# Optimization experiments

Hardware: AMD Instinct MI355X
Metric: run time of the kernel (lower is better)

The kernel has to match this reference:

```python
import jax, jax.numpy as jnp
import numpy as np
from math import factorial

MAXL = 5
TAUS = [8, 8, 8, 8, 8, 8]
OUT_TAUS = [8, 8, 8, 8, 8, 8]
BM_EPS = 1e-5
BATCH = 1024


def _cg_coeff(l1, l2, l, m1, m2, m):
    # Standard Clebsch-Gordan coefficient <l1 m1 l2 m2 | l m> (Racah formula).
    if m1 + m2 != m:
        return 0.0
    f = factorial
    pre = ((2 * l + 1) * f(l + l1 - l2) * f(l - l1 + l2) * f(l1 + l2 - l) / f(l1 + l2 + l + 1)) ** 0.5
    pre *= (f(l + m) * f(l - m) * f(l1 - m1) * f(l1 + m1) * f(l2 - m2) * f(l2 + m2)) ** 0.5
    s = 0.0
    for k in range(0, l1 + l2 - l + 1):
        ds = [k, l1 + l2 - l - k, l1 - m1 - k, l2 + m2 - k, l - l2 + m1 + k, l - l1 - m2 + k]
        if min(ds) < 0:
            continue
        d = 1.0
        for v in ds:
            d *= f(v)
        s += (-1.0) ** k / d
    return pre * s


def _cg_block(l1, l2, l):
    C = np.zeros((2 * l + 1, 2 * l1 + 1, 2 * l2 + 1), dtype=np.float32)
    for m in range(-l, l + 1):
        for m1 in range(-l1, l1 + 1):
            m2 = m - m1
            if -l2 <= m2 <= l2:
                C[m + l, m1 + l1, m2 + l2] = _cg_coeff(l1, l2, l, m1, m2, m)
    return C


# Triple enumeration order matches cal_middle_taus (l1 outer, l2, then l).
TRIPLES = []
for _l1 in range(MAXL + 1):
    for _l2 in range(_l1 + 1):
        for _l in range(_l1 - _l2, min(_l1 + _l2, MAXL) + 1):
            TRIPLES.append((_l1, _l2, _l))
CG_BLOCKS = [jnp.asarray(_cg_block(*t)) for t in TRIPLES]

MIDDLE_TAUS = np.zeros(MAXL + 1, dtype=np.int64)
for (_l1, _l2, _l) in TRIPLES:
    MIDDLE_TAUS[_l] += TAUS[_l1] * TAUS[_l2]
IN_LEN = int(sum(TAUS[l] * (2 * l + 1) for l in range(MAXL + 1)))    # 288
OUT_LEN = int(sum(OUT_TAUS[l] * (2 * l + 1) for l in range(MAXL + 1)))  # 288
WLEN = int(sum(OUT_TAUS[l] * int(MIDDLE_TAUS[l]) for l in range(MAXL + 1)))  # 35328
STD_LEN = int(MIDDLE_TAUS.sum())  # 4416


def _forward(activations, weights, moving_std):
    B = activations.shape[0]
    act = activations[..., 0] + 1j * activations[..., 1]  # [B, IN_LEN] complex64
    # split into per-degree blocks F[l]: [B, tau_l, 2l+1]
    F = []
    st = 0
    for l in range(MAXL + 1):
        n = TAUS[l] * (2 * l + 1)
        F.append(act[:, st:st + n].reshape(B, TAUS[l], 2 * l + 1))
        st += n
    # CG tensor product: one fragment per (l1,l2,l) triple, grouped by output degree l
    mids = [[] for _ in range(MAXL + 1)]
    for (l1, l2, l), C in zip(TRIPLES, CG_BLOCKS):
        frag = jnp.einsum('mac,bta,bsc->btsm', C.astype(act.dtype), F[l1], F[l2])
        mids[l].append(frag.reshape(B, TAUS[l1] * TAUS[l2], 2 * l + 1))
    # per-fragment batchnorm (divide by running std) + per-degree complex mixing
    outs = []
    so = 0
    wo = 0
    for l in range(MAXL + 1):
        mid = jnp.concatenate(mids[l], axis=1)  # [B, middle_taus[l], 2l+1]
        nt = int(MIDDLE_TAUS[l])
        std = moving_std[so:so + nt]
        so += nt
        mid = mid / (std + BM_EPS)[None, :, None]
        nw = OUT_TAUS[l] * nt
        wl = weights[wo:wo + nw]
        wo += nw
        Wc = (wl[:, 0] + 1j * wl[:, 1]).reshape(OUT_TAUS[l], nt)
        out = jnp.einsum('ot,btm->bom', Wc, mid)  # [B, out_taus[l], 2l+1]
        outs.append(out.reshape(B, OUT_TAUS[l] * (2 * l + 1)))
    oc = jnp.concatenate(outs, axis=1)  # [B, OUT_LEN] complex
    return jnp.stack([oc.real, oc.imag], axis=-1)  # [B, OUT_LEN, 2]


def setup_inputs() -> dict:
    key = jax.random.key(0)
    k1, k2, k3 = jax.random.split(key, 3)
    activations = jax.random.normal(k1, (BATCH, IN_LEN, 2), dtype=jnp.float32)
    weights = 0.05 * jax.random.uniform(k2, (WLEN, 2), dtype=jnp.float32)
    moving_std = 0.1 + 0.9 * jax.random.uniform(k3, (STD_LEN,), dtype=jnp.float32)
    return {"activations": activations, "weights": weights, "moving_std": moving_std}


def reference(activations, weights, moving_std):
    return _forward(activations, weights, moving_std)
```

## Files before the change

### kernel.cpp

```cpp
#include <hip/hip_runtime.h>
#include <hip/hip_bf16.h>
#include <utility>


constexpr int NTRIP = 69;
constexpr int NL    = 6;
constexpr int BATCH = 1024;
constexpr int ROW   = 288;
constexpr int MID_LDS = 4224;

struct Meta {
    int tl1[NTRIP], tl2[NTRIP], tll[NTRIP];
    int tf1[NTRIP], tf2[NTRIP];
    int ttloc[NTRIP];
    int trip_of_l[NL][16];
    int ntrips[NL];
    int mid_tau[NL], std_off[NL], w_off[NL], f_l[NL];
    int nch[NL];
    int ch_start[NL][2], ch_cnt[NL][2];
    int wave_of[NL][16];
};

constexpr Meta build_meta() {
    Meta m{};
    int fl[NL] = {};
    {
        int acc = 0;
        for (int l = 0; l < NL; l++) { fl[l] = acc; m.f_l[l] = acc; acc += 8 * (2 * l + 1); }
    }
    int idx = 0;
    for (int l1 = 0; l1 <= 5; l1++)
        for (int l2 = 0; l2 <= l1; l2++) {
            int lmax = (l1 + l2 < 5) ? (l1 + l2) : 5;
            for (int l = l1 - l2; l <= lmax; l++) {
                m.tl1[idx] = l1; m.tl2[idx] = l2; m.tll[idx] = l;
                m.tf1[idx] = fl[l1]; m.tf2[idx] = fl[l2];
                m.ttloc[idx] = 64 * m.ntrips[l];
                m.trip_of_l[l][m.ntrips[l]] = idx;
                m.ntrips[l]++;
                idx++;
            }
        }
    int so = 0, wo = 0;
    for (int l = 0; l < NL; l++) {
        m.mid_tau[l] = 64 * m.ntrips[l];
        m.std_off[l] = so; so += m.mid_tau[l];
        m.w_off[l]   = wo; wo += 8 * m.mid_tau[l];
    }
    for (int l = 0; l < NL; l++) {
        const int TW = 2 * l + 1;
        const int maxslot = MID_LDS / (64 * TW);
        const int ntl = m.ntrips[l];
        const int nch = (ntl + maxslot - 1) / maxslot;
        m.nch[l] = nch;
        int done = 0;
        for (int c = 0; c < nch; c++) {
            int cnt = (ntl - done + (nch - c) - 1) / (nch - c);
            m.ch_start[l][c] = done; m.ch_cnt[l][c] = cnt; done += cnt;
        }
        for (int c = 0; c < nch; c++) {
            const int s0 = m.ch_start[l][c], cnt = m.ch_cnt[l][c];
            int cost[16] = {}; bool asg[16] = {};
            for (int i = 0; i < cnt; i++) {
                int trip = m.trip_of_l[l][s0 + i];
                int l1 = m.tl1[trip], l2 = m.tl2[trip];
                int tc = 0;
                for (int mi = 0; mi < TW; mi++) {
                    int base = mi - l;
                    int lo = base + l1 - l2; if (lo < 0) lo = 0;
                    int hi = base + l1 + l2; if (hi > 2 * l1) hi = 2 * l1;
                    tc += hi - lo + 1;
                }
                cost[i] = tc * 6 + (2 * l1 + 1 + 2 * l2 + 1) * 2;
            }
            int load[4] = {};
            for (int k = 0; k < cnt; k++) {
                int best = -1, bc = -1;
                for (int i = 0; i < cnt; i++)
                    if (!asg[i] && cost[i] > bc) { bc = cost[i]; best = i; }
                asg[best] = true;
                int wsel = 0;
                for (int w2 = 1; w2 < 4; w2++) if (load[w2] < load[wsel]) wsel = w2;
                m.wave_of[l][s0 + best] = wsel;
                load[wsel] += bc;
            }
        }
    }
    return m;
}

constexpr Meta MT = build_meta();
constexpr int WLEN = 35328;
static_assert(MT.w_off[5] + 8 * MT.mid_tau[5] == WLEN, "wlen");
static_assert(MT.std_off[5] + MT.mid_tau[5] == 4416, "stdlen");

constexpr double cfact(int n) {
    double r = 1.0;
    for (int i = 2; i <= n; i++) r *= (double)i;
    return r;
}
constexpr double csqrt(double x) {
    double g = x > 1.0 ? x : 1.0;
    for (int i = 0; i < 100; i++) g = 0.5 * (g + x / g);
    return g;
}
constexpr float cg_coeff(int l1, int l2, int l, int m1, int m2, int m) {
    if (m1 + m2 != m) return 0.0f;
    double pre = csqrt((double)(2 * l + 1) * cfact(l + l1 - l2) * cfact(l - l1 + l2) *
                       cfact(l1 + l2 - l) / cfact(l1 + l2 + l + 1));
    pre *= csqrt(cfact(l + m) * cfact(l - m) * cfact(l1 - m1) * cfact(l1 + m1) *
                 cfact(l2 - m2) * cfact(l2 + m2));
    double s = 0.0;
    for (int k = 0; k <= l1 + l2 - l; k++) {
        int d0 = k, d1 = l1 + l2 - l - k, d2 = l1 - m1 - k;
        int d3 = l2 + m2 - k, d4 = l - l2 + m1 + k, d5 = l - l1 - m2 + k;
        if (d0 < 0 || d1 < 0 || d2 < 0 || d3 < 0 || d4 < 0 || d5 < 0) continue;
        double den = cfact(d0) * cfact(d1) * cfact(d2) * cfact(d3) * cfact(d4) * cfact(d5);
        s += ((k & 1) ? -1.0 : 1.0) / den;
    }
    return (float)(pre * s);
}

template <int... Is, class F>
__device__ __forceinline__ void static_for_impl(std::integer_sequence<int, Is...>, F&& f) {
    (f(std::integral_constant<int, Is>{}), ...);
}
template <int N, class F>
__device__ __forceinline__ void static_for(F&& f) {
    static_for_impl(std::make_integer_sequence<int, N>{}, (F&&)f);
}

__global__ void w_init(const float2* __restrict__ w,
                       const float* __restrict__ stdv,
                       float2* __restrict__ wp) {
    int i = blockIdx.x * 256 + threadIdx.x;
    if (i >= WLEN) return;
    int l = 0;
    for (int k = 1; k < NL; k++) if (MT.w_off[k] <= i) l = k;
    int rel = i - MT.w_off[l];
    int T = rel % MT.mid_tau[l];
    float inv = 1.0f / (stdv[MT.std_off[l] + T] + 1e-5f);
    float2 wv = w[i];
    wp[i] = make_float2(wv.x * inv, wv.y * inv);
}

template <int L>
__device__ __forceinline__ void process_l(int b, int tid,
                                          const float2* __restrict__ F,
                                          float2* __restrict__ mid,
                                          const float2* __restrict__ wp,
                                          float2* __restrict__ out) {
    constexpr int TW  = 2 * L + 1;
    constexpr int NCH = MT.nch[L];
    constexpr int NT  = MT.mid_tau[L];

    const int wid  = tid >> 6;
    const int lane = tid & 63;
    const int t = lane >> 3, s = lane & 7;

    float2 acc0[TW], acc1[TW];
#pragma unroll
    for (int i = 0; i < TW; i++) { acc0[i] = make_float2(0.f, 0.f); acc1[i] = make_float2(0.f, 0.f); }

    static_for<NCH>([&](auto CHc) {
        constexpr int CH  = decltype(CHc)::value;
        constexpr int S0  = MT.ch_start[L][CH];
        constexpr int CNT = MT.ch_cnt[L][CH];
        constexpr int CT  = CNT * 64;
        static_assert(CT * TW <= MID_LDS, "chunk fits");

        __syncthreads();

        static_for<CNT>([&](auto SIc) {
            constexpr int SI   = S0 + decltype(SIc)::value;
            constexpr int TRIP = MT.trip_of_l[L][SI];
            constexpr int L1   = MT.tl1[TRIP];
            constexpr int L2v  = MT.tl2[TRIP];
            constexpr int N1   = 2 * L1 + 1, N2 = 2 * L2v + 1;
            if (MT.wave_of[L][SI] == wid) {
                const float2* F1 = F + MT.tf1[TRIP] + t * N1;
                const float2* F2 = F + MT.tf2[TRIP] + s * N2;
                float2 f1[N1], f2[N2];
#pragma unroll
                for (int i = 0; i < N1; i++) f1[i] = F1[i];
#pragma unroll
                for (int i = 0; i < N2; i++) f2[i] = F2[i];
                const int Tloc = (MT.ttloc[TRIP] - S0 * 64) + lane;
                static_for<TW>([&](auto MIc) {
                    constexpr int MI   = decltype(MIc)::value;
                    constexpr int BASE = MI - L;
                    constexpr int LO_  = BASE + L1 - L2v;
                    constexpr int LO   = LO_ < 0 ? 0 : LO_;
                    constexpr int HI_  = BASE + L1 + L2v;
                    constexpr int HI   = HI_ > 2 * L1 ? 2 * L1 : HI_;
                    float re = 0.f, im = 0.f;
                    static_for<HI - LO + 1>([&](auto Kc) {
                        constexpr int AI = LO + decltype(Kc)::value;
                        constexpr int CI = BASE + L1 + L2v - AI;
                        constexpr float cv = cg_coeff(L1, L2v, L, AI - L1, CI - L2v, BASE);
                        if constexpr (cv != 0.0f) {
                            const float2 a = f1[AI], c2 = f2[CI];
                            re = fmaf(cv, fmaf(-a.y, c2.y, a.x * c2.x), re);
                            im = fmaf(cv, fmaf(a.y, c2.x, a.x * c2.y), im);
                        }
                    });
                    mid[MI * CT + Tloc] = make_float2(re, im);
                });
            }
        });
        __syncthreads();

        const float2* W0 = wp + MT.w_off[L] + wid * NT + S0 * 64;
        const float2* W1 = wp + MT.w_off[L] + (wid + 4) * NT + S0 * 64;
        for (int T = lane * 2; T < CT; T += 128) {
            const float4 w0 = *reinterpret_cast<const float4*>(W0 + T);
            const float4 w1 = *reinterpret_cast<const float4*>(W1 + T);
#pragma unroll
            for (int mi = 0; mi < TW; mi++) {
                const float4 mv = *reinterpret_cast<const float4*>(mid + mi * CT + T);
                acc0[mi].x = fmaf(w0.x, mv.x, fmaf(-w0.y, mv.y,
                              fmaf(w0.z, mv.z, fmaf(-w0.w, mv.w, acc0[mi].x))));
                acc0[mi].y = fmaf(w0.x, mv.y, fmaf(w0.y, mv.x,
                              fmaf(w0.z, mv.w, fmaf(w0.w, mv.z, acc0[mi].y))));
                acc1[mi].x = fmaf(w1.x, mv.x, fmaf(-w1.y, mv.y,
                              fmaf(w1.z, mv.z, fmaf(-w1.w, mv.w, acc1[mi].x))));
                acc1[mi].y = fmaf(w1.x, mv.y, fmaf(w1.y, mv.x,
                              fmaf(w1.z, mv.w, fmaf(w1.w, mv.z, acc1[mi].y))));
            }
        }
    });

    const bool lo = (lane < 32);
    float2 red[TW];
#pragma unroll
    for (int mi = 0; mi < TW; mi++) {
        float gx = lo ? acc1[mi].x : acc0[mi].x;
        float gy = lo ? acc1[mi].y : acc0[mi].y;
        float rx = (lo ? acc0[mi].x : acc1[mi].x) + __shfl_xor(gx, 32, 64);
        float ry = (lo ? acc0[mi].y : acc1[mi].y) + __shfl_xor(gy, 32, 64);
#pragma unroll
        for (int off = 16; off >= 1; off >>= 1) {
            rx += __shfl_xor(rx, off, 64);
            ry += __shfl_xor(ry, off, 64);
        }
        red[mi] = make_float2(rx, ry);
    }
    if (lane == 0 || lane == 32) {
        const int o = wid + (lo ? 0 : 4);
        float2* orow = out + (size_t)b * ROW + MT.f_l[L] + o * TW;
#pragma unroll
        for (int mi = 0; mi < TW; mi++) orow[mi] = red[mi];
    }
}

__global__ __launch_bounds__(256, 4) void fup_main(const float2* __restrict__ act,
                                                   const float2* __restrict__ wp,
                                                   float2* __restrict__ out) {
    __shared__ float2 F[ROW];
    __shared__ __align__(16) float2 mid[MID_LDS];
    const int b = blockIdx.x;
    const int tid = threadIdx.x;
    const float2* arow = act + (size_t)b * ROW;
    for (int i = tid; i < ROW; i += 256) F[i] = arow[i];
    process_l<0>(b, tid, F, mid, wp, out);
    process_l<1>(b, tid, F, mid, wp, out);
    process_l<2>(b, tid, F, mid, wp, out);
    process_l<3>(b, tid, F, mid, wp, out);
    process_l<4>(b, tid, F, mid, wp, out);
    process_l<5>(b, tid, F, mid, wp, out);
}

extern "C" void kernel_launch(void* const* d_in, const int* in_sizes, int n_in,
                              void* d_out, int out_size, void* d_ws, size_t ws_size,
                              hipStream_t stream) {
    const float2* act  = (const float2*)d_in[0];
    const float2* wts  = (const float2*)d_in[1];
    const float*  stdv = (const float*)d_in[2];
    float2* out = (float2*)d_out;

    float2* wp = (float2*)d_ws;

    hipLaunchKernelGGL(w_init, dim3((WLEN + 255) / 256), dim3(256), 0, stream,
                       wts, stdv, wp);
    hipLaunchKernelGGL(fup_main, dim3(BATCH), dim3(256), 0, stream, act, wp, out);
}
```

Before: 114.8 us.

## Double-buffer mid chunks, prefetch weights, fold std scaling into main kernel

Splits the mid buffer into two smaller LDS halves and software-pipelines the work: while one chunk is contracted with the weights, the next chunk's CG products are computed and its weights are prefetched into registers. This drops one barrier per chunk. The per-channel 1/std scaling moves from a separate weight-prep kernel onto the mid values, which removes a launch and a workspace round trip. In exchange there are more, smaller chunks (15 in total), each CG thread recomputes the reciprocal, and the register arrays used for prefetch raise register pressure.

```diff
diff --git a/kernel.cpp b/kernel.cpp
--- a/kernel.cpp
+++ b/kernel.cpp
@@ -7,7 +7,8 @@
 constexpr int NL    = 6;
 constexpr int BATCH = 1024;
 constexpr int ROW   = 288;
-constexpr int MID_LDS = 4224;
+constexpr int MIDB  = 2368;
+constexpr int NCHK  = 15;
 
 struct Meta {
     int tl1[NTRIP], tl2[NTRIP], tll[NTRIP];
@@ -17,8 +18,10 @@
     int ntrips[NL];
     int mid_tau[NL], std_off[NL], w_off[NL], f_l[NL];
     int nch[NL];
-    int ch_start[NL][2], ch_cnt[NL][2];
+    int ch_start[NL][8], ch_cnt[NL][8];
     int wave_of[NL][16];
+    int ck_l[NCHK], ck_s0[NCHK], ck_cnt[NCHK];
+    int ck_first[NL];
 };
 
 constexpr Meta build_meta() {
@@ -49,7 +52,7 @@
     }
     for (int l = 0; l < NL; l++) {
         const int TW = 2 * l + 1;
-        const int maxslot = MID_LDS / (64 * TW);
+        const int maxslot = MIDB / (64 * TW);
         const int ntl = m.ntrips[l];
         const int nch = (ntl + maxslot - 1) / maxslot;
         m.nch[l] = nch;
@@ -86,6 +89,14 @@
             }
         }
     }
+    int ci = 0;
+    for (int l = 0; l < NL; l++) {
+        m.ck_first[l] = ci;
+        for (int c = 0; c < m.nch[l]; c++) {
+            m.ck_l[ci] = l; m.ck_s0[ci] = m.ch_start[l][c]; m.ck_cnt[ci] = m.ch_cnt[l][c];
+            ci++;
+        }
+    }
     return m;
 }
 
@@ -93,6 +104,7 @@
 constexpr int WLEN = 35328;
 static_assert(MT.w_off[5] + 8 * MT.mid_tau[5] == WLEN, "wlen");
 static_assert(MT.std_off[5] + MT.mid_tau[5] == 4416, "stdlen");
+static_assert(MT.ck_first[5] + MT.nch[5] == NCHK, "nchk");
 
 constexpr double cfact(int n) {
     double r = 1.0;
@@ -130,91 +142,107 @@
     static_for_impl(std::make_integer_sequence<int, N>{}, (F&&)f);
 }
 
-__global__ void w_init(const float2* __restrict__ w,
-                       const float* __restrict__ stdv,
-                       float2* __restrict__ wp) {
-    int i = blockIdx.x * 256 + threadIdx.x;
-    if (i >= WLEN) return;
-    int l = 0;
-    for (int k = 1; k < NL; k++) if (MT.w_off[k] <= i) l = k;
-    int rel = i - MT.w_off[l];
-    int T = rel % MT.mid_tau[l];
-    float inv = 1.0f / (stdv[MT.std_off[l] + T] + 1e-5f);
-    float2 wv = w[i];
-    wp[i] = make_float2(wv.x * inv, wv.y * inv);
-}
-
-template <int L>
-__device__ __forceinline__ void process_l(int b, int tid,
-                                          const float2* __restrict__ F,
-                                          float2* __restrict__ mid,
-                                          const float2* __restrict__ wp,
-                                          float2* __restrict__ out) {
+__device__ __forceinline__ void barrier_lgkm() {
+    asm volatile("s_waitcnt lgkmcnt(0)\n\ts_barrier" ::: "memory");
+}
+
+template <int C>
+__device__ __forceinline__ void s1_chunk(const int tid,
+                                         const float2* __restrict__ F,
+                                         float2* __restrict__ midb,
+                                         const float2* __restrict__ w,
+                                         const float* __restrict__ stdv,
+                                         float4 (&wA)[5], float4 (&wB)[5]) {
+    constexpr int L   = MT.ck_l[C];
+    constexpr int S0  = MT.ck_s0[C];
+    constexpr int CNT = MT.ck_cnt[C];
     constexpr int TW  = 2 * L + 1;
-    constexpr int NCH = MT.nch[L];
+    constexpr int CT  = CNT * 64;
     constexpr int NT  = MT.mid_tau[L];
-
+    static_assert(CT * TW <= MIDB, "chunk fits");
+    float2* mid = midb + (C & 1) * MIDB;
     const int wid  = tid >> 6;
     const int lane = tid & 63;
     const int t = lane >> 3, s = lane & 7;
 
-    float2 acc0[TW], acc1[TW];
-#pragma unroll
-    for (int i = 0; i < TW; i++) { acc0[i] = make_float2(0.f, 0.f); acc1[i] = make_float2(0.f, 0.f); }
-
-    static_for<NCH>([&](auto CHc) {
-        constexpr int CH  = decltype(CHc)::value;
-        constexpr int S0  = MT.ch_start[L][CH];
-        constexpr int CNT = MT.ch_cnt[L][CH];
-        constexpr int CT  = CNT * 64;
-        static_assert(CT * TW <= MID_LDS, "chunk fits");
-
-        __syncthreads();
-
-        static_for<CNT>([&](auto SIc) {
-            constexpr int SI   = S0 + decltype(SIc)::value;
-            constexpr int TRIP = MT.trip_of_l[L][SI];
-            constexpr int L1   = MT.tl1[TRIP];
-            constexpr int L2v  = MT.tl2[TRIP];
-            constexpr int N1   = 2 * L1 + 1, N2 = 2 * L2v + 1;
-            if (MT.wave_of[L][SI] == wid) {
-                const float2* F1 = F + MT.tf1[TRIP] + t * N1;
-                const float2* F2 = F + MT.tf2[TRIP] + s * N2;
-                float2 f1[N1], f2[N2];
-#pragma unroll
-                for (int i = 0; i < N1; i++) f1[i] = F1[i];
-#pragma unroll
-                for (int i = 0; i < N2; i++) f2[i] = F2[i];
-                const int Tloc = (MT.ttloc[TRIP] - S0 * 64) + lane;
-                static_for<TW>([&](auto MIc) {
-                    constexpr int MI   = decltype(MIc)::value;
-                    constexpr int BASE = MI - L;
-                    constexpr int LO_  = BASE + L1 - L2v;
-                    constexpr int LO   = LO_ < 0 ? 0 : LO_;
-                    constexpr int HI_  = BASE + L1 + L2v;
-                    constexpr int HI   = HI_ > 2 * L1 ? 2 * L1 : HI_;
-                    float re = 0.f, im = 0.f;
-                    static_for<HI - LO + 1>([&](auto Kc) {
-                        constexpr int AI = LO + decltype(Kc)::value;
-                        constexpr int CI = BASE + L1 + L2v - AI;
-                        constexpr float cv = cg_coeff(L1, L2v, L, AI - L1, CI - L2v, BASE);
-                        if constexpr (cv != 0.0f) {
-                            const float2 a = f1[AI], c2 = f2[CI];
-                            re = fmaf(cv, fmaf(-a.y, c2.y, a.x * c2.x), re);
-                            im = fmaf(cv, fmaf(a.y, c2.x, a.x * c2.y), im);
-                        }
-                    });
-                    mid[MI * CT + Tloc] = make_float2(re, im);
+    constexpr int NIT = (CT + 127) / 128;
+    static_assert(NIT <= 5, "prefetch depth");
+    {
+        const float2* W0 = w + MT.w_off[L] + wid * NT + S0 * 64;
+        const float2* W1 = w + MT.w_off[L] + (wid + 4) * NT + S0 * 64;
+        static_for<NIT>([&](auto Ic) {
+            constexpr int I = decltype(Ic)::value;
+            const int T = lane * 2 + I * 128;
+            if constexpr ((I + 1) * 128 <= CT) {
+                wA[I] = *reinterpret_cast<const float4*>(W0 + T);
+                wB[I] = *reinterpret_cast<const float4*>(W1 + T);
+            } else {
+                if (T < CT) {
+                    wA[I] = *reinterpret_cast<const float4*>(W0 + T);
+                    wB[I] = *reinterpret_cast<const float4*>(W1 + T);
+                }
+            }
+        });
+    }
+
+    static_for<CNT>([&](auto SIc) {
+        constexpr int SI   = S0 + decltype(SIc)::value;
+        constexpr int TRIP = MT.trip_of_l[L][SI];
+        constexpr int L1   = MT.tl1[TRIP];
+        constexpr int L2v  = MT.tl2[TRIP];
+        constexpr int N1   = 2 * L1 + 1, N2 = 2 * L2v + 1;
+        if (MT.wave_of[L][SI] == wid) {
+            const float inv = 1.0f /
+                (stdv[MT.std_off[L] + MT.ttloc[TRIP] + lane] + 1e-5f);
+            const float2* F1 = F + MT.tf1[TRIP] + t * N1;
+            const float2* F2 = F + MT.tf2[TRIP] + s * N2;
+            float2 f1[N1], f2[N2];
+#pragma unroll
+            for (int i = 0; i < N1; i++) f1[i] = F1[i];
+#pragma unroll
+            for (int i = 0; i < N2; i++) f2[i] = F2[i];
+            const int Tloc = (MT.ttloc[TRIP] - S0 * 64) + lane;
+            static_for<TW>([&](auto MIc) {
+                constexpr int MI   = decltype(MIc)::value;
+                constexpr int BASE = MI - L;
+                constexpr int LO_  = BASE + L1 - L2v;
+                constexpr int LO   = LO_ < 0 ? 0 : LO_;
+                constexpr int HI_  = BASE + L1 + L2v;
+                constexpr int HI   = HI_ > 2 * L1 ? 2 * L1 : HI_;
+                float re = 0.f, im = 0.f;
+                static_for<HI - LO + 1>([&](auto Kc) {
+                    constexpr int AI = LO + decltype(Kc)::value;
+                    constexpr int CI = BASE + L1 + L2v - AI;
+                    constexpr float cv = cg_coeff(L1, L2v, L, AI - L1, CI - L2v, BASE);
+                    if constexpr (cv != 0.0f) {
+                        const float2 a = f1[AI], c2 = f2[CI];
+                        re = fmaf(cv, fmaf(-a.y, c2.y, a.x * c2.x), re);
+                        im = fmaf(cv, fmaf(a.y, c2.x, a.x * c2.y), im);
+                    }
                 });
-            }
-        });
-        __syncthreads();
-
-        const float2* W0 = wp + MT.w_off[L] + wid * NT + S0 * 64;
-        const float2* W1 = wp + MT.w_off[L] + (wid + 4) * NT + S0 * 64;
-        for (int T = lane * 2; T < CT; T += 128) {
-            const float4 w0 = *reinterpret_cast<const float4*>(W0 + T);
-            const float4 w1 = *reinterpret_cast<const float4*>(W1 + T);
+                mid[MI * CT + Tloc] = make_float2(re * inv, im * inv);
+            });
+        }
+    });
+}
+
+template <int C, int TW>
+__device__ __forceinline__ void s2_chunk(const int tid,
+                                         const float2* __restrict__ midb,
+                                         float2 (&acc0)[TW], float2 (&acc1)[TW],
+                                         const float4 (&wA)[5], const float4 (&wB)[5]) {
+    constexpr int L  = MT.ck_l[C];
+    static_assert(TW == 2 * L + 1, "tw");
+    constexpr int CT = MT.ck_cnt[C] * 64;
+    constexpr int NIT = (CT + 127) / 128;
+    const float2* mid = midb + (C & 1) * MIDB;
+    const int lane = tid & 63;
+
+    static_for<NIT>([&](auto Ic) {
+        constexpr int I = decltype(Ic)::value;
+        const int T = lane * 2 + I * 128;
+        const float4 w0 = wA[I], w1 = wB[I];
+        auto body = [&]() {
 #pragma unroll
             for (int mi = 0; mi < TW; mi++) {
                 const float4 mv = *reinterpret_cast<const float4*>(mid + mi * CT + T);
@@ -227,7 +255,36 @@
                 acc1[mi].y = fmaf(w1.x, mv.y, fmaf(w1.y, mv.x,
                               fmaf(w1.z, mv.w, fmaf(w1.w, mv.z, acc1[mi].y))));
             }
-        }
+        };
+        if constexpr ((I + 1) * 128 <= CT) body();
+        else { if (T < CT) body(); }
+    });
+}
+
+template <int L>
+__device__ __forceinline__ void process_l(const int b, const int tid,
+                                          const float2* __restrict__ F,
+                                          float2* __restrict__ midb,
+                                          const float2* __restrict__ w,
+                                          const float* __restrict__ stdv,
+                                          float2* __restrict__ out,
+                                          float4 (&wA)[5], float4 (&wB)[5]) {
+    constexpr int TW = 2 * L + 1;
+    constexpr int NC = MT.nch[L];
+    constexpr int C0 = MT.ck_first[L];
+    const int wid  = tid >> 6;
+    const int lane = tid & 63;
+
+    float2 acc0[TW], acc1[TW];
+#pragma unroll
+    for (int i = 0; i < TW; i++) { acc0[i] = make_float2(0.f, 0.f); acc1[i] = make_float2(0.f, 0.f); }
+
+    static_for<NC>([&](auto Cc) {
+        constexpr int C = C0 + decltype(Cc)::value;
+        barrier_lgkm();
+        s2_chunk<C, TW>(tid, midb, acc0, acc1, wA, wB);
+        if constexpr (C + 1 < NCHK)
+            s1_chunk<C + 1>(tid, F, midb, w, stdv, wA, wB);
     });
 
     const bool lo = (lane < 32);
@@ -254,20 +311,25 @@
 }
 
 __global__ __launch_bounds__(256, 4) void fup_main(const float2* __restrict__ act,
-                                                   const float2* __restrict__ wp,
+                                                   const float2* __restrict__ w,
+                                                   const float* __restrict__ stdv,
                                                    float2* __restrict__ out) {
     __shared__ float2 F[ROW];
-    __shared__ __align__(16) float2 mid[MID_LDS];
+    __shared__ __align__(16) float2 midb[2 * MIDB];
     const int b = blockIdx.x;
     const int tid = threadIdx.x;
     const float2* arow = act + (size_t)b * ROW;
     for (int i = tid; i < ROW; i += 256) F[i] = arow[i];
-    process_l<0>(b, tid, F, mid, wp, out);
-    process_l<1>(b, tid, F, mid, wp, out);
-    process_l<2>(b, tid, F, mid, wp, out);
-    process_l<3>(b, tid, F, mid, wp, out);
-    process_l<4>(b, tid, F, mid, wp, out);
-    process_l<5>(b, tid, F, mid, wp, out);
+
+    float4 wA[5], wB[5];
+    __syncthreads();
+    s1_chunk<0>(tid, F, midb, w, stdv, wA, wB);
+    process_l<0>(b, tid, F, midb, w, stdv, out, wA, wB);
+    process_l<1>(b, tid, F, midb, w, stdv, out, wA, wB);
+    process_l<2>(b, tid, F, midb, w, stdv, out, wA, wB);
+    process_l<3>(b, tid, F, midb, w, stdv, out, wA, wB);
+    process_l<4>(b, tid, F, midb, w, stdv, out, wA, wB);
+    process_l<5>(b, tid, F, midb, w, stdv, out, wA, wB);
 }
 
 extern "C" void kernel_launch(void* const* d_in, const int* in_sizes, int n_in,
@@ -277,10 +339,8 @@
     const float2* wts  = (const float2*)d_in[1];
     const float*  stdv = (const float*)d_in[2];
     float2* out = (float2*)d_out;
-
-    float2* wp = (float2*)d_ws;
-
-    hipLaunchKernelGGL(w_init, dim3((WLEN + 255) / 256), dim3(256), 0, stream,
-                       wts, stdv, wp);
-    hipLaunchKernelGGL(fup_main, dim3(BATCH), dim3(256), 0, stream, act, wp, out);
-}
+    (void)d_ws; (void)ws_size;
+
+    hipLaunchKernelGGL(fup_main, dim3(BATCH), dim3(256), 0, stream,
+                       act, wts, stdv, out);
+}
```

Measured after the change: 297.4 us. 159% more time.

## Fold moving-std normalization into mid computation and drop weight prep kernel

Applied to the files above, without the earlier changes.

Removes the separate w_init kernel that pre-scaled the weights by 1/(std+eps). The main kernel now multiplies each mid value by the reciprocal std when writing it to LDS and reads the raw weights directly. It also hoists all weight float4 loads for a chunk into registers before the FMA loop, so global loads can be issued early. This saves one kernel launch and a weight write/read round trip, at the cost of one extra std load and reciprocal per mid element in every block and higher register pressure.

```diff
diff --git a/kernel.cpp b/kernel.cpp
--- a/kernel.cpp
+++ b/kernel.cpp
@@ -130,25 +130,12 @@
     static_for_impl(std::make_integer_sequence<int, N>{}, (F&&)f);
 }
 
-__global__ void w_init(const float2* __restrict__ w,
-                       const float* __restrict__ stdv,
-                       float2* __restrict__ wp) {
-    int i = blockIdx.x * 256 + threadIdx.x;
-    if (i >= WLEN) return;
-    int l = 0;
-    for (int k = 1; k < NL; k++) if (MT.w_off[k] <= i) l = k;
-    int rel = i - MT.w_off[l];
-    int T = rel % MT.mid_tau[l];
-    float inv = 1.0f / (stdv[MT.std_off[l] + T] + 1e-5f);
-    float2 wv = w[i];
-    wp[i] = make_float2(wv.x * inv, wv.y * inv);
-}
-
 template <int L>
 __device__ __forceinline__ void process_l(int b, int tid,
                                           const float2* __restrict__ F,
                                           float2* __restrict__ mid,
-                                          const float2* __restrict__ wp,
+                                          const float2* __restrict__ w,
+                                          const float* __restrict__ stdv,
                                           float2* __restrict__ out) {
     constexpr int TW  = 2 * L + 1;
     constexpr int NCH = MT.nch[L];
@@ -178,6 +165,8 @@
             constexpr int L2v  = MT.tl2[TRIP];
             constexpr int N1   = 2 * L1 + 1, N2 = 2 * L2v + 1;
             if (MT.wave_of[L][SI] == wid) {
+                const float inv = 1.0f /
+                    (stdv[MT.std_off[L] + MT.ttloc[TRIP] + lane] + 1e-5f);
                 const float2* F1 = F + MT.tf1[TRIP] + t * N1;
                 const float2* F2 = F + MT.tf2[TRIP] + s * N2;
                 float2 f1[N1], f2[N2];
@@ -204,29 +193,51 @@
                             im = fmaf(cv, fmaf(a.y, c2.x, a.x * c2.y), im);
                         }
                     });
-                    mid[MI * CT + Tloc] = make_float2(re, im);
+                    mid[MI * CT + Tloc] = make_float2(re * inv, im * inv);
                 });
             }
         });
         __syncthreads();
 
-        const float2* W0 = wp + MT.w_off[L] + wid * NT + S0 * 64;
-        const float2* W1 = wp + MT.w_off[L] + (wid + 4) * NT + S0 * 64;
-        for (int T = lane * 2; T < CT; T += 128) {
-            const float4 w0 = *reinterpret_cast<const float4*>(W0 + T);
-            const float4 w1 = *reinterpret_cast<const float4*>(W1 + T);
-#pragma unroll
-            for (int mi = 0; mi < TW; mi++) {
-                const float4 mv = *reinterpret_cast<const float4*>(mid + mi * CT + T);
-                acc0[mi].x = fmaf(w0.x, mv.x, fmaf(-w0.y, mv.y,
-                              fmaf(w0.z, mv.z, fmaf(-w0.w, mv.w, acc0[mi].x))));
-                acc0[mi].y = fmaf(w0.x, mv.y, fmaf(w0.y, mv.x,
-                              fmaf(w0.z, mv.w, fmaf(w0.w, mv.z, acc0[mi].y))));
-                acc1[mi].x = fmaf(w1.x, mv.x, fmaf(-w1.y, mv.y,
-                              fmaf(w1.z, mv.z, fmaf(-w1.w, mv.w, acc1[mi].x))));
-                acc1[mi].y = fmaf(w1.x, mv.y, fmaf(w1.y, mv.x,
-                              fmaf(w1.z, mv.w, fmaf(w1.w, mv.z, acc1[mi].y))));
-            }
+        {
+            constexpr int NIT = (CT + 127) / 128;
+            const float2* W0 = w + MT.w_off[L] + wid * NT + S0 * 64;
+            const float2* W1 = w + MT.w_off[L] + (wid + 4) * NT + S0 * 64;
+            float4 wA[NIT], wB[NIT];
+            static_for<NIT>([&](auto Ic) {
+                constexpr int I = decltype(Ic)::value;
+                const int T = lane * 2 + I * 128;
+                if constexpr ((I + 1) * 128 <= CT) {
+                    wA[I] = *reinterpret_cast<const float4*>(W0 + T);
+                    wB[I] = *reinterpret_cast<const float4*>(W1 + T);
+                } else {
+                    if (T < CT) {
+                        wA[I] = *reinterpret_cast<const float4*>(W0 + T);
+                        wB[I] = *reinterpret_cast<const float4*>(W1 + T);
+                    }
+                }
+            });
+            static_for<NIT>([&](auto Ic) {
+                constexpr int I = decltype(Ic)::value;
+                const int T = lane * 2 + I * 128;
+                const float4 w0 = wA[I], w1 = wB[I];
+                auto body = [&]() {
+#pragma unroll
+                    for (int mi = 0; mi < TW; mi++) {
+                        const float4 mv = *reinterpret_cast<const float4*>(mid + mi * CT + T);
+                        acc0[mi].x = fmaf(w0.x, mv.x, fmaf(-w0.y, mv.y,
+                                      fmaf(w0.z, mv.z, fmaf(-w0.w, mv.w, acc0[mi].x))));
+                        acc0[mi].y = fmaf(w0.x, mv.y, fmaf(w0.y, mv.x,
+                                      fmaf(w0.z, mv.w, fmaf(w0.w, mv.z, acc0[mi].y))));
+                        acc1[mi].x = fmaf(w1.x, mv.x, fmaf(-w1.y, mv.y,
+                                      fmaf(w1.z, mv.z, fmaf(-w1.w, mv.w, acc1[mi].x))));
+                        acc1[mi].y = fmaf(w1.x, mv.y, fmaf(w1.y, mv.x,
+                                      fmaf(w1.z, mv.w, fmaf(w1.w, mv.z, acc1[mi].y))));
+                    }
+                };
+                if constexpr ((I + 1) * 128 <= CT) body();
+                else { if (T < CT) body(); }
+            });
         }
     });
 
@@ -254,7 +265,8 @@
 }
 
 __global__ __launch_bounds__(256, 4) void fup_main(const float2* __restrict__ act,
-                                                   const float2* __restrict__ wp,
+                                                   const float2* __restrict__ w,
+                                                   const float* __restrict__ stdv,
                                                    float2* __restrict__ out) {
     __shared__ float2 F[ROW];
     __shared__ __align__(16) float2 mid[MID_LDS];
@@ -262,12 +274,12 @@
     const int tid = threadIdx.x;
     const float2* arow = act + (size_t)b * ROW;
     for (int i = tid; i < ROW; i += 256) F[i] = arow[i];
-    process_l<0>(b, tid, F, mid, wp, out);
-    process_l<1>(b, tid, F, mid, wp, out);
-    process_l<2>(b, tid, F, mid, wp, out);
-    process_l<3>(b, tid, F, mid, wp, out);
-    process_l<4>(b, tid, F, mid, wp, out);
-    process_l<5>(b, tid, F, mid, wp, out);
+    process_l<0>(b, tid, F, mid, w, stdv, out);
+    process_l<1>(b, tid, F, mid, w, stdv, out);
+    process_l<2>(b, tid, F, mid, w, stdv, out);
+    process_l<3>(b, tid, F, mid, w, stdv, out);
+    process_l<4>(b, tid, F, mid, w, stdv, out);
+    process_l<5>(b, tid, F, mid, w, stdv, out);
 }
 
 extern "C" void kernel_launch(void* const* d_in, const int* in_sizes, int n_in,
@@ -277,10 +289,8 @@
     const float2* wts  = (const float2*)d_in[1];
     const float*  stdv = (const float*)d_in[2];
     float2* out = (float2*)d_out;
-
-    float2* wp = (float2*)d_ws;
-
-    hipLaunchKernelGGL(w_init, dim3((WLEN + 255) / 256), dim3(256), 0, stream,
-                       wts, stdv, wp);
-    hipLaunchKernelGGL(fup_main, dim3(BATCH), dim3(256), 0, stream, act, wp, out);
-}
+    (void)d_ws; (void)ws_size;
+
+    hipLaunchKernelGGL(fup_main, dim3(BATCH), dim3(256), 0, stream,
+                       act, wts, stdv, out);
+}
```

New measurement: 138.2 us. 1.2x slower.
